# Kernel optimization log

Measured on AMD Instinct MI355X. Metric: run time of the kernel, lower is better.

## Reference

```python
import jax, jax.numpy as jnp
import numpy as np

RES = (256, 256)
FLOW_TEMP_REG = 1e-3
LOSS_SCALING = True
EPS = 1e-9


def get_interpolation(events, flow, tref, res):
    # events: [B,N,4] (ts,y,x,p); flow: [B,N,2] per-event (flow_y, flow_x)
    warped = events[:, :, 1:3] + (tref - events[:, :, 0:1]) * flow  # [B,N,2] (y,x)
    top_y = jnp.floor(warped[:, :, 0:1])
    bot_y = top_y + 1.0
    left_x = jnp.floor(warped[:, :, 1:2])
    right_x = left_x + 1.0
    # four bilinear corners stacked along the event dim -> [B,4N,2]
    idx = jnp.concatenate([
        jnp.concatenate([top_y, left_x], axis=2),
        jnp.concatenate([top_y, right_x], axis=2),
        jnp.concatenate([bot_y, left_x], axis=2),
        jnp.concatenate([bot_y, right_x], axis=2)], axis=1)
    w = jnp.maximum(0.0, 1.0 - jnp.abs(jnp.tile(warped, (1, 4, 1)) - idx))  # [B,4N,2]
    mask = ((idx[:, :, 0:1] >= 0) & (idx[:, :, 0:1] < res[0]) &
            (idx[:, :, 1:2] >= 0) & (idx[:, :, 1:2] < res[1])).astype(w.dtype)
    idx = idx * mask  # out-of-bounds -> pixel 0 with zero weight
    w = w * mask
    flat_idx = (idx[:, :, 0] * res[1] + idx[:, :, 1]).astype(jnp.int32)  # [B,4N]
    weights = w[:, :, 0] * w[:, :, 1]  # bilinear weight, [B,4N]
    return flat_idx, weights


def interpolate(flat_idx, w, npix):
    # per-batch scatter-add of weights into a flat pixel grid -> [B, H*W]
    return jax.vmap(lambda i, v: jax.ops.segment_sum(v, i, num_segments=npix))(flat_idx, w)


def scale_loss(iwe_pos, iwe_neg, iwe_pos_ts, iwe_neg_ts):
    loss = jnp.sum(iwe_pos_ts ** 2, axis=1) + jnp.sum(iwe_neg_ts ** 2, axis=1)  # [B]
    if LOSS_SCALING:
        nonzero_px = jnp.sum(((iwe_pos + iwe_neg) != 0).astype(loss.dtype), axis=1)
        loss = loss / (nonzero_px + EPS)
    return jnp.sum(loss)


def forward(event_list, flow, pol_mask, vector_list, max_ts):
    res = RES
    npix = res[0] * res[1]
    mt = jnp.asarray(max_ts, jnp.float32)
    pm = jnp.tile(pol_mask, (1, 4, 1))                    # [B,4N,2]
    ts4 = jnp.tile(event_list[:, :, 0], (1, 4))           # [B,4N]
    loss = jnp.float32(0.0)
    # forward warp (tref=max_ts, weight ts) and backward warp (tref=0, weight max_ts-ts)
    for tref, ts_w in ((mt, ts4), (jnp.float32(0.0), mt - ts4)):
        idx, w = get_interpolation(event_list, flow, tref, res)
        wp = w * pm[:, :, 0]
        wn = w * pm[:, :, 1]
        iwe_pos = interpolate(idx, wp, npix)
        iwe_neg = interpolate(idx, wn, npix)
        iwe_pos_ts = interpolate(idx, wp * ts_w, npix) / (iwe_pos + EPS) / mt
        iwe_neg_ts = interpolate(idx, wn * ts_w, npix) / (iwe_neg + EPS) / mt
        loss = loss + scale_loss(iwe_pos, iwe_neg, iwe_pos_ts, iwe_neg_ts)
    # single flow scale in _flow_list -> divide by 1
    loss = loss / 1.0
    # Charbonnier temporal smoothness on flow vectors [B,P,8]
    dt = vector_list[:, :-1, :] - vector_list[:, 1:, :]
    dt = jnp.sqrt(dt ** 2 + EPS).reshape(vector_list.shape[0], -1)
    loss = loss + FLOW_TEMP_REG * jnp.sum(jnp.mean(dt, axis=1))
    return loss


def setup_inputs() -> dict:
    B, N, P = 8, 262144, 4
    H, W = RES
    key = jax.random.key(0)
    ks = jax.random.split(key, 6)
    ts = jax.random.uniform(ks[0], (B, N, 1), dtype=jnp.float32) * P
    y = jax.random.uniform(ks[1], (B, N, 1), dtype=jnp.float32) * (H - 1)
    x = jax.random.uniform(ks[2], (B, N, 1), dtype=jnp.float32) * (W - 1)
    p = jax.random.bernoulli(ks[3], 0.5, (B, N, 1)).astype(jnp.float32) * 2.0 - 1.0
    event_list = jnp.concatenate([ts, y, x, p], axis=2)
    pos = (p > 0).astype(jnp.float32)
    pol_mask = jnp.concatenate([pos, 1.0 - pos], axis=2)
    flow = jax.random.normal(ks[4], (B, N, 2), dtype=jnp.float32) * 2.0
    vector_list = jax.random.normal(ks[5], (B, P, 8), dtype=jnp.float32)
    return {"event_list": event_list, "flow": flow, "pol_mask": pol_mask,
            "vector_list": vector_list, "max_ts": P}


def reference(event_list, flow, pol_mask, vector_list, max_ts):
    return forward(event_list, flow, pol_mask, vector_list, max_ts)
```

## Files before the change

kernel.cpp:

```cpp
#include <hip/hip_runtime.h>
#include <math.h>

#define RES_H 256
#define RES_W 256
#define NPIX 65536
#define EPSF 1e-9f
#define FLOW_TEMP_REG 1e-3f

#define N_BANDS 8
#define BAND_ROWS 32
#define BAND_PX (BAND_ROWS * RES_W)
#define N_CHUNKS 2
#define CAP 49152
#define QS 2048.0f
#define QINV (1.0f / 2048.0f)
#define EV_PER_BLOCK 2048
#define EV_PER_THREAD 8

#define PAD 32

typedef unsigned long long u64;
typedef unsigned int u32;

__device__ __forceinline__ float decode_mt(const int* p) {
    int raw = *p;
    if (raw >= 0 && raw < (1 << 23)) return (float)raw;
    union { int i; float f; } u; u.i = raw; return u.f;
}


__global__ void __launch_bounds__(256) ew_bin(
    const float4* __restrict__ ev, const float2* __restrict__ flow,
    const int* __restrict__ mt_ptr, u64* __restrict__ recs,
    u32* __restrict__ counts, int N)
{
    __shared__ u32 hist[16], basebuf[16], cursor[16];
    const int b = blockIdx.y;
    const int start = blockIdx.x * EV_PER_BLOCK;
    const int tid = threadIdx.x;
    if (tid < 16) { hist[tid] = 0u; cursor[tid] = 0u; }
    __syncthreads();

    const float mt = decode_mt(mt_ptr);
    const float inv_mt = 1.0f / mt;

    float4 e[EV_PER_THREAD];
    float2 f[EV_PER_THREAD];
    #pragma unroll
    for (int j = 0; j < EV_PER_THREAD; ++j) {
        int i = start + tid + j * 256;
        if (i < N) { e[j] = ev[b * N + i]; f[j] = flow[b * N + i]; }
        else { e[j] = make_float4(0.f, -100.f, -100.f, 1.f); f[j] = make_float2(0.f, 0.f); }
    }

    #pragma unroll
    for (int j = 0; j < EV_PER_THREAD; ++j) {
        #pragma unroll
        for (int dir = 0; dir < 2; ++dir) {
            float dtt = (dir ? 0.0f : mt) - e[j].x;
            float wy = fminf(fmaxf(e[j].y + dtt * f[j].x, -8.0f), 264.0f);
            float wx = fminf(fmaxf(e[j].z + dtt * f[j].y, -8.0f), 264.0f);
            int wyf = __float2int_rn(wy * 4096.0f);
            int wxf = __float2int_rn(wx * 4096.0f);
            int iy = wyf >> 12, ix = wxf >> 12;
            if (iy < -1 || iy > 255 || ix < -1 || ix > 255) continue;
            int t1 = iy >> 5;
            int t2 = (iy + 1) >> 5;
            if (t1 >= 0) atomicAdd(&hist[dir * 8 + t1], 1u);
            if (t2 <= 7 && t2 != t1) atomicAdd(&hist[dir * 8 + t2], 1u);
        }
    }
    __syncthreads();
    if (tid < 16) basebuf[tid] = atomicAdd(&counts[(b * 16 + tid) * PAD], hist[tid]);
    __syncthreads();

    #pragma unroll
    for (int j = 0; j < EV_PER_THREAD; ++j) {
        #pragma unroll
        for (int dir = 0; dir < 2; ++dir) {
            float dtt = (dir ? 0.0f : mt) - e[j].x;
            float tswn = (dir ? (mt - e[j].x) : e[j].x) * inv_mt;
            float wy = fminf(fmaxf(e[j].y + dtt * f[j].x, -8.0f), 264.0f);
            float wx = fminf(fmaxf(e[j].z + dtt * f[j].y, -8.0f), 264.0f);
            int wyf = __float2int_rn(wy * 4096.0f);
            int wxf = __float2int_rn(wx * 4096.0f);
            int iy = wyf >> 12, ix = wxf >> 12;
            if (iy < -1 || iy > 255 || ix < -1 || ix > 255) continue;
            u32 tq = __float2uint_rn(fminf(fmaxf(tswn, 0.0f), 1.0f) * 4096.0f);
            u64 rec = (u64)((u32)wyf & 0x3FFFFFu)
                    | ((u64)((u32)wxf & 0x3FFFFFu) << 22)
                    | ((u64)tq << 44)
                    | ((u64)(e[j].w > 0.0f ? 0u : 1u) << 57);
            int t1 = iy >> 5;
            int t2 = (iy + 1) >> 5;
            #pragma unroll
            for (int s = 0; s < 2; ++s) {
                int t = s ? t2 : t1;
                if (t < 0 || t > 7) continue;
                if (s && t2 == t1) continue;
                int k = dir * 8 + t;
                u32 off = atomicAdd(&cursor[k], 1u);
                u32 slot = basebuf[k] + off;
                if (slot >= CAP) slot = CAP - 1;
                recs[(size_t)(b * 16 + k) * CAP + slot] = rec;
            }
        }
    }
}

__global__ void __launch_bounds__(1024) ew_accum(
    const u64* __restrict__ recs, const u32* __restrict__ counts,
    u32* __restrict__ accum)
{
    __shared__ u32 lds[2 * BAND_PX];
    const int band = blockIdx.x, bd = blockIdx.y, c = blockIdx.z;
    const int q = bd * 8 + band;
    const int row0 = band * BAND_ROWS;
    for (int i = threadIdx.x; i < 2 * BAND_PX; i += 1024) lds[i] = 0u;
    __syncthreads();

    u32 cnt = counts[q * PAD]; if (cnt > CAP) cnt = CAP;
    u32 lo = cnt * (u32)c / N_CHUNKS;
    u32 hi = cnt * (u32)(c + 1) / N_CHUNKS;
    const u64* bucket = recs + (size_t)q * CAP;

    for (u32 i = lo + threadIdx.x; i < hi; i += 1024) {
        u64 rec = bucket[i];
        int wyf = ((int)(((u32)rec & 0x3FFFFFu) << 10)) >> 10;
        int wxf = ((int)(((u32)(rec >> 22) & 0x3FFFFFu) << 10)) >> 10;
        float tswn = (float)((u32)(rec >> 44) & 0x1FFFu) * (1.0f / 4096.0f);
        u32 pol = (u32)(rec >> 57) & 1u;
        int ry = (wyf >> 12) - row0;
        int ix = wxf >> 12;
        float fy = (float)(wyf & 0xFFF) * (1.0f / 4096.0f);
        float fx = (float)(wxf & 0xFFF) * (1.0f / 4096.0f);
        u32* pl = lds + pol * BAND_PX;
        #pragma unroll
        for (int cc = 0; cc < 4; ++cc) {
            int cy = ry + (cc >> 1), cx = ix + (cc & 1);
            if ((unsigned)cy >= BAND_ROWS || (unsigned)cx >= RES_W) continue;
            float wgt = ((cc >> 1) ? fy : 1.0f - fy) * ((cc & 1) ? fx : 1.0f - fx);
            u32 v = (__float2uint_rn(wgt * tswn * QS) << 16)
                  |  __float2uint_rn(wgt * QS);
            if (v) atomicAdd(&pl[(cy << 8) | cx], v);
        }
    }
    __syncthreads();

    u32* out0 = accum + ((size_t)(c * 16 + bd) * 2) * NPIX + row0 * RES_W;
    for (int i = threadIdx.x; i < BAND_PX; i += 1024) {
        out0[i]        = lds[i];
        out0[NPIX + i] = lds[BAND_PX + i];
    }
}

__global__ void __launch_bounds__(256) ew_reduce(
    const u32* __restrict__ accum, float* __restrict__ partials)
{
    const int bd  = blockIdx.y;
    const int tid = threadIdx.x;
    const int i4  = blockIdx.x * 256 + tid;

    const uint4 c0p = ((const uint4*)(accum + (((size_t)(0 * 16 + bd) * 2 + 0) << 16)))[i4];
    const uint4 c0n = ((const uint4*)(accum + (((size_t)(0 * 16 + bd) * 2 + 1) << 16)))[i4];
    const uint4 c1p = ((const uint4*)(accum + (((size_t)(1 * 16 + bd) * 2 + 0) << 16)))[i4];
    const uint4 c1n = ((const uint4*)(accum + (((size_t)(1 * 16 + bd) * 2 + 1) << 16)))[i4];

    float term = 0.0f, nz = 0.0f;
    const u32 pu[4] = {c0p.x, c0p.y, c0p.z, c0p.w};
    const u32 nu[4] = {c0n.x, c0n.y, c0n.z, c0n.w};
    const u32 pv[4] = {c1p.x, c1p.y, c1p.z, c1p.w};
    const u32 nv[4] = {c1n.x, c1n.y, c1n.z, c1n.w};
    #pragma unroll
    for (int j = 0; j < 4; ++j) {
        u32 wp_r = (pu[j] & 0xFFFFu) + (pv[j] & 0xFFFFu);
        u32 tp_r = (pu[j] >> 16)     + (pv[j] >> 16);
        u32 wn_r = (nu[j] & 0xFFFFu) + (nv[j] & 0xFFFFu);
        u32 tn_r = (nu[j] >> 16)     + (nv[j] >> 16);
        float wp = (float)wp_r * QINV, tp = (float)tp_r * QINV;
        float wn = (float)wn_r * QINV, tn = (float)tn_r * QINV;
        float pts = tp / (wp + EPSF);
        float nts = tn / (wn + EPSF);
        term += pts * pts + nts * nts;
        nz   += ((wp_r | wn_r) != 0u) ? 1.0f : 0.0f;
    }

    #pragma unroll
    for (int off = 32; off > 0; off >>= 1) {
        term += __shfl_down(term, off);
        nz   += __shfl_down(nz, off);
    }
    __shared__ float wterm[4], wnz[4];
    if ((tid & 63) == 0) { wterm[tid >> 6] = term; wnz[tid >> 6] = nz; }
    __syncthreads();
    if (tid == 0) {
        float t = wterm[0] + wterm[1] + wterm[2] + wterm[3];
        float z = wnz[0] + wnz[1] + wnz[2] + wnz[3];
        atomicAdd(&partials[bd * PAD + 0], t);
        atomicAdd(&partials[bd * PAD + 1], z);
    }
}

__global__ void __launch_bounds__(256) ew_finalize(
    const float* __restrict__ partials, const float* __restrict__ vec,
    float* __restrict__ out, int B, int P, int n_bd)
{
    int tid = threadIdx.x;
    float v = 0.0f;
    if (tid < n_bd) {
        float s = partials[tid * PAD + 0];
        float n = partials[tid * PAD + 1];
        v = s / (n + EPSF);
    }
    int per_b = (P - 1) * 8;
    int total = B * per_b;
    float sm = 0.0f;
    for (int i = tid; i < total; i += blockDim.x) {
        int b = i / per_b;
        int r = i - b * per_b;
        int pi = r >> 3, j = r & 7;
        float d = vec[(b * P + pi) * 8 + j] - vec[(b * P + pi + 1) * 8 + j];
        sm += sqrtf(d * d + EPSF);
    }
    sm = sm / (float)per_b * FLOW_TEMP_REG;

    __shared__ float sdata[256];
    sdata[tid] = v + sm;
    __syncthreads();
    for (int s = 128; s > 0; s >>= 1) {
        if (tid < s) sdata[tid] += sdata[tid + s];
        __syncthreads();
    }
    if (tid == 0) out[0] = sdata[0];
}

extern "C" void kernel_launch(void* const* d_in, const int* in_sizes, int n_in,
                              void* d_out, int out_size, void* d_ws, size_t ws_size,
                              hipStream_t stream) {
    const float4* ev   = (const float4*)d_in[0];
    const float2* flow = (const float2*)d_in[1];
    const float*  vec  = (const float*)d_in[3];
    const int*    mtp  = (const int*)d_in[4];

    const int B = 8;
    const int N = in_sizes[0] / (B * 4);
    const int P = in_sizes[3] / (B * 8);

    u32*   counts   = (u32*)d_ws;
    float* partials = (float*)((char*)d_ws + 65536);
    u32*   accum    = (u32*)((char*)d_ws + 131072);
    size_t accum_bytes = (size_t)N_CHUNKS * 16 * 2 * NPIX * sizeof(u32);
    u64*   recs     = (u64*)((char*)d_ws + 131072 + accum_bytes);

    hipMemsetAsync(d_ws, 0, 131072, stream);

    dim3 bgrid((N + EV_PER_BLOCK - 1) / EV_PER_BLOCK, B);
    ew_bin<<<bgrid, 256, 0, stream>>>(ev, flow, mtp, recs, counts, N);

    dim3 agrid(N_BANDS, 16, N_CHUNKS);
    ew_accum<<<agrid, 1024, 0, stream>>>(recs, counts, accum);

    dim3 rgrid(64, 16);
    ew_reduce<<<rgrid, 256, 0, stream>>>(accum, partials);

    ew_finalize<<<1, 256, 0, stream>>>(partials, vec, (float*)d_out, B, P, 16);
}
```

Measured before the change: 132.6 us.

## Fuse pixel reduction into banded LDS accumulation and use finer row bands

```diff
diff --git a/kernel.cpp b/kernel.cpp
--- a/kernel.cpp
+++ b/kernel.cpp
@@ -7,11 +7,11 @@
 #define EPSF 1e-9f
 #define FLOW_TEMP_REG 1e-3f
 
-#define N_BANDS 8
-#define BAND_ROWS 32
+#define BAND_SHIFT 4
+#define BAND_ROWS 16
+#define N_BANDS 16
 #define BAND_PX (BAND_ROWS * RES_W)
-#define N_CHUNKS 2
-#define CAP 49152
+#define CAP 24576
 #define QS 2048.0f
 #define QINV (1.0f / 2048.0f)
 #define EV_PER_BLOCK 2048
@@ -34,11 +34,11 @@
     const int* __restrict__ mt_ptr, u64* __restrict__ recs,
     u32* __restrict__ counts, int N)
 {
-    __shared__ u32 hist[16], basebuf[16], cursor[16];
+    __shared__ u32 hist[32], basebuf[32], cursor[32];
     const int b = blockIdx.y;
     const int start = blockIdx.x * EV_PER_BLOCK;
     const int tid = threadIdx.x;
-    if (tid < 16) { hist[tid] = 0u; cursor[tid] = 0u; }
+    if (tid < 32) { hist[tid] = 0u; cursor[tid] = 0u; }
     __syncthreads();
 
     const float mt = decode_mt(mt_ptr);
@@ -64,14 +64,14 @@
             int wxf = __float2int_rn(wx * 4096.0f);
             int iy = wyf >> 12, ix = wxf >> 12;
             if (iy < -1 || iy > 255 || ix < -1 || ix > 255) continue;
-            int t1 = iy >> 5;
-            int t2 = (iy + 1) >> 5;
-            if (t1 >= 0) atomicAdd(&hist[dir * 8 + t1], 1u);
-            if (t2 <= 7 && t2 != t1) atomicAdd(&hist[dir * 8 + t2], 1u);
+            int t1 = iy >> BAND_SHIFT;
+            int t2 = (iy + 1) >> BAND_SHIFT;
+            if (t1 >= 0) atomicAdd(&hist[dir * 16 + t1], 1u);
+            if (t2 <= 15 && t2 != t1) atomicAdd(&hist[dir * 16 + t2], 1u);
         }
     }
     __syncthreads();
-    if (tid < 16) basebuf[tid] = atomicAdd(&counts[(b * 16 + tid) * PAD], hist[tid]);
+    if (tid < 32) basebuf[tid] = atomicAdd(&counts[(b * 32 + tid) * PAD], hist[tid]);
     __syncthreads();
 
     #pragma unroll
@@ -91,18 +91,18 @@
                     | ((u64)((u32)wxf & 0x3FFFFFu) << 22)
                     | ((u64)tq << 44)
                     | ((u64)(e[j].w > 0.0f ? 0u : 1u) << 57);
-            int t1 = iy >> 5;
-            int t2 = (iy + 1) >> 5;
+            int t1 = iy >> BAND_SHIFT;
+            int t2 = (iy + 1) >> BAND_SHIFT;
             #pragma unroll
             for (int s = 0; s < 2; ++s) {
                 int t = s ? t2 : t1;
-                if (t < 0 || t > 7) continue;
+                if (t < 0 || t > 15) continue;
                 if (s && t2 == t1) continue;
-                int k = dir * 8 + t;
+                int k = dir * 16 + t;
                 u32 off = atomicAdd(&cursor[k], 1u);
                 u32 slot = basebuf[k] + off;
                 if (slot >= CAP) slot = CAP - 1;
-                recs[(size_t)(b * 16 + k) * CAP + slot] = rec;
+                recs[(size_t)(b * 32 + k) * CAP + slot] = rec;
             }
         }
     }
@@ -110,21 +110,21 @@
 
 __global__ void __launch_bounds__(1024) ew_accum(
     const u64* __restrict__ recs, const u32* __restrict__ counts,
-    u32* __restrict__ accum)
+    float* __restrict__ partials)
 {
     __shared__ u32 lds[2 * BAND_PX];
-    const int band = blockIdx.x, bd = blockIdx.y, c = blockIdx.z;
-    const int q = bd * 8 + band;
-    const int row0 = band * BAND_ROWS;
-    for (int i = threadIdx.x; i < 2 * BAND_PX; i += 1024) lds[i] = 0u;
+    __shared__ float wterm[16], wnz[16];
+    const int band = blockIdx.x, bd = blockIdx.y;
+    const int q = bd * 16 + band;
+    const int row0 = band << BAND_SHIFT;
+    const int tid = threadIdx.x;
+    for (int i = tid; i < 2 * BAND_PX; i += 1024) lds[i] = 0u;
     __syncthreads();
 
     u32 cnt = counts[q * PAD]; if (cnt > CAP) cnt = CAP;
-    u32 lo = cnt * (u32)c / N_CHUNKS;
-    u32 hi = cnt * (u32)(c + 1) / N_CHUNKS;
     const u64* bucket = recs + (size_t)q * CAP;
 
-    for (u32 i = lo + threadIdx.x; i < hi; i += 1024) {
+    for (u32 i = tid; i < cnt; i += 1024) {
         u64 rec = bucket[i];
         int wyf = ((int)(((u32)rec & 0x3FFFFFu) << 10)) >> 10;
         int wxf = ((int)(((u32)(rec >> 22) & 0x3FFFFFu) << 10)) >> 10;
@@ -147,36 +147,15 @@
     }
     __syncthreads();
 
-    u32* out0 = accum + ((size_t)(c * 16 + bd) * 2) * NPIX + row0 * RES_W;
-    for (int i = threadIdx.x; i < BAND_PX; i += 1024) {
-        out0[i]        = lds[i];
-        out0[NPIX + i] = lds[BAND_PX + i];
-    }
-}
-
-__global__ void __launch_bounds__(256) ew_reduce(
-    const u32* __restrict__ accum, float* __restrict__ partials)
-{
-    const int bd  = blockIdx.y;
-    const int tid = threadIdx.x;
-    const int i4  = blockIdx.x * 256 + tid;
-
-    const uint4 c0p = ((const uint4*)(accum + (((size_t)(0 * 16 + bd) * 2 + 0) << 16)))[i4];
-    const uint4 c0n = ((const uint4*)(accum + (((size_t)(0 * 16 + bd) * 2 + 1) << 16)))[i4];
-    const uint4 c1p = ((const uint4*)(accum + (((size_t)(1 * 16 + bd) * 2 + 0) << 16)))[i4];
-    const uint4 c1n = ((const uint4*)(accum + (((size_t)(1 * 16 + bd) * 2 + 1) << 16)))[i4];
-
+    const uint4 pp = ((const uint4*)lds)[tid];
+    const uint4 nn = ((const uint4*)(lds + BAND_PX))[tid];
+    const u32 pu[4] = {pp.x, pp.y, pp.z, pp.w};
+    const u32 nu[4] = {nn.x, nn.y, nn.z, nn.w};
     float term = 0.0f, nz = 0.0f;
-    const u32 pu[4] = {c0p.x, c0p.y, c0p.z, c0p.w};
-    const u32 nu[4] = {c0n.x, c0n.y, c0n.z, c0n.w};
-    const u32 pv[4] = {c1p.x, c1p.y, c1p.z, c1p.w};
-    const u32 nv[4] = {c1n.x, c1n.y, c1n.z, c1n.w};
     #pragma unroll
     for (int j = 0; j < 4; ++j) {
-        u32 wp_r = (pu[j] & 0xFFFFu) + (pv[j] & 0xFFFFu);
-        u32 tp_r = (pu[j] >> 16)     + (pv[j] >> 16);
-        u32 wn_r = (nu[j] & 0xFFFFu) + (nv[j] & 0xFFFFu);
-        u32 tn_r = (nu[j] >> 16)     + (nv[j] >> 16);
+        u32 wp_r = pu[j] & 0xFFFFu, tp_r = pu[j] >> 16;
+        u32 wn_r = nu[j] & 0xFFFFu, tn_r = nu[j] >> 16;
         float wp = (float)wp_r * QINV, tp = (float)tp_r * QINV;
         float wn = (float)wn_r * QINV, tn = (float)tn_r * QINV;
         float pts = tp / (wp + EPSF);
@@ -184,18 +163,17 @@
         term += pts * pts + nts * nts;
         nz   += ((wp_r | wn_r) != 0u) ? 1.0f : 0.0f;
     }
-
     #pragma unroll
     for (int off = 32; off > 0; off >>= 1) {
         term += __shfl_down(term, off);
         nz   += __shfl_down(nz, off);
     }
-    __shared__ float wterm[4], wnz[4];
     if ((tid & 63) == 0) { wterm[tid >> 6] = term; wnz[tid >> 6] = nz; }
     __syncthreads();
     if (tid == 0) {
-        float t = wterm[0] + wterm[1] + wterm[2] + wterm[3];
-        float z = wnz[0] + wnz[1] + wnz[2] + wnz[3];
+        float t = 0.0f, z = 0.0f;
+        #pragma unroll
+        for (int wv = 0; wv < 16; ++wv) { t += wterm[wv]; z += wnz[wv]; }
         atomicAdd(&partials[bd * PAD + 0], t);
         atomicAdd(&partials[bd * PAD + 1], z);
     }
@@ -247,21 +225,16 @@
     const int P = in_sizes[3] / (B * 8);
 
     u32*   counts   = (u32*)d_ws;
-    float* partials = (float*)((char*)d_ws + 65536);
-    u32*   accum    = (u32*)((char*)d_ws + 131072);
-    size_t accum_bytes = (size_t)N_CHUNKS * 16 * 2 * NPIX * sizeof(u32);
-    u64*   recs     = (u64*)((char*)d_ws + 131072 + accum_bytes);
-
-    hipMemsetAsync(d_ws, 0, 131072, stream);
+    float* partials = (float*)((char*)d_ws + 32768);
+    u64*   recs     = (u64*)((char*)d_ws + 65536);
+
+    hipMemsetAsync(d_ws, 0, 65536, stream);
 
     dim3 bgrid((N + EV_PER_BLOCK - 1) / EV_PER_BLOCK, B);
     ew_bin<<<bgrid, 256, 0, stream>>>(ev, flow, mtp, recs, counts, N);
 
-    dim3 agrid(N_BANDS, 16, N_CHUNKS);
-    ew_accum<<<agrid, 1024, 0, stream>>>(recs, counts, accum);
-
-    dim3 rgrid(64, 16);
-    ew_reduce<<<rgrid, 256, 0, stream>>>(accum, partials);
+    dim3 agrid(N_BANDS, 16);
+    ew_accum<<<agrid, 1024, 0, stream>>>(recs, counts, partials);
 
     ew_finalize<<<1, 256, 0, stream>>>(partials, vec, (float*)d_out, B, P, 16);
 }
```

Measured after the change: 127.1 us. -4.2%, faster.
